# Kernel optimization log

Hardware: AMD Instinct MI355X
Metric: run time of the kernel (lower is better)

The kernel has to match this reference:

```python
import jax, jax.numpy as jnp
import numpy as np

D_MODEL = 512
H = 8
DEPTH = D_MODEL // H
TOPK = 16
TAU_HID = max(4, D_MODEL // 2)  # 256
TAU_EPS = 1e-6
DT = 1.0
T_SCALAR = 1.0  # default t in call()


def setup_inputs() -> dict:
    key = jax.random.key(0)
    ks = jax.random.split(key, 24)
    B, T = 2, 1024
    D2 = 2 * DEPTH

    def w(k, shape, fan_in):
        return jax.random.normal(k, shape, dtype=jnp.float32) / np.sqrt(fan_in)

    inp = {
        "x": jax.random.normal(ks[0], (B, T, D_MODEL), dtype=jnp.float32),
        "Wq": w(ks[1], (D_MODEL, D_MODEL), D_MODEL), "bq": jnp.zeros((D_MODEL,), jnp.float32),
        "Wk": w(ks[2], (D_MODEL, D_MODEL), D_MODEL), "bk": jnp.zeros((D_MODEL,), jnp.float32),
        "Wv": w(ks[3], (D_MODEL, D_MODEL), D_MODEL), "bv": jnp.zeros((D_MODEL,), jnp.float32),
        "Wo": w(ks[4], (D_MODEL, D_MODEL), D_MODEL), "bo": jnp.zeros((D_MODEL,), jnp.float32),
        "Wpi": w(ks[5], (D2, D_MODEL), D2), "bpi": jnp.zeros((D_MODEL,), jnp.float32),
        "Wpo": w(ks[6], (D_MODEL, 1), D_MODEL), "bpo": jnp.zeros((1,), jnp.float32),
        "Wta": w(ks[7], (D2, 1), D2), "bta": jnp.zeros((1,), jnp.float32),
        "Wtb": w(ks[8], (D2, 1), D2), "btb": jnp.zeros((1,), jnp.float32),
        "Wti": w(ks[9], (D2, TAU_HID), D2), "bti": jnp.zeros((TAU_HID,), jnp.float32),
        "Wto": w(ks[10], (TAU_HID, 1), TAU_HID), "bto": jnp.zeros((1,), jnp.float32),
    }
    return inp


def reference(x, Wq, bq, Wk, bk, Wv, bv, Wo, bo,
              Wpi, bpi, Wpo, bpo, Wta, bta, Wtb, btb, Wti, bti, Wto, bto):
    B, T, _ = x.shape

    def split_heads(z):
        return z.reshape(B, T, H, DEPTH).transpose(0, 2, 1, 3)  # [B,H,T,D]

    qh = split_heads(x @ Wq + bq)
    kh = split_heads(x @ Wk + bk)
    vh = split_heads(x @ Wv + bv)

    # top-k pairwise scores (q @ k^T), select K keys per query
    scores = jnp.einsum('bhqd,bhkd->bhqk', qh, kh)  # [B,H,T,T]
    _, idx = jax.lax.top_k(scores, TOPK)            # [B,H,T,K]

    # gather k and v at top-k indices -> [B,H,T,K,D]
    kg = jnp.take_along_axis(kh[:, :, None, :, :], idx[..., None], axis=3)
    vg = jnp.take_along_axis(vh[:, :, None, :, :], idx[..., None], axis=3)

    # per-pair features [q_i ; k_j] -> [B,H,T,K,2D]
    qt = jnp.broadcast_to(qh[:, :, :, None, :], (B, H, T, TOPK, DEPTH))
    pairs = jnp.concatenate([qt, kg], axis=-1)

    # phi: Dense(d_model) -> Dense(1) -> sigmoid
    phi = jax.nn.sigmoid(((pairs @ Wpi + bpi) @ Wpo + bpo)[..., 0])
    # time interpolation: sigmoid(a*t + b)
    t_a = (pairs @ Wta + bta)[..., 0]
    t_b = (pairs @ Wtb + btb)[..., 0]
    t_interp = jax.nn.sigmoid(t_a * T_SCALAR + t_b)
    # tau: Dense(d_model//2) -> Dense(1) -> softplus + eps
    tau = jax.nn.softplus(((pairs @ Wti + bti) @ Wto + bto)[..., 0]) + TAU_EPS

    # mode == 'exact'
    attn_logits = phi / tau * (1.0 - jnp.exp(-tau * t_interp))
    attn = jax.nn.softmax(attn_logits, axis=-1)  # [B,H,T,K]

    out_h = jnp.einsum('bhqk,bhqkd->bhqd', attn, vg) * DT  # [B,H,T,D]
    combined = out_h.transpose(0, 2, 1, 3).reshape(B, T, D_MODEL)
    return combined @ Wo + bo  # return_sequences=True
```

## Files before the change

### kernel.cpp

```cpp
#include <hip/hip_runtime.h>
#include <math.h>

#define BDIM 2
#define TT 1024
#define NH 8
#define HD 64
#define NTOPK 16
#define NBH 16
#define NTOK 16384

__global__ __launch_bounds__(256) void k_collapse64(
    const float* __restrict__ Wpi, const float* __restrict__ bpi,
    const float* __restrict__ Wpo, const float* __restrict__ bpo,
    const float* __restrict__ Wti, const float* __restrict__ bti,
    const float* __restrict__ Wto, const float* __restrict__ bto,
    double* __restrict__ wphid, double* __restrict__ wtaud,
    double* __restrict__ ccd) {
  int tid = threadIdx.x;
  int blk = blockIdx.x;
  if (blk < 16) {
    int r = blk * 16 + (tid >> 4);
    int l = tid & 15;
    double s = 0.;
    if (r < 128) {
      for (int i = 0; i < 32; ++i)
        s += (double)Wpi[r * 512 + l + 16 * i] * (double)Wpo[l + 16 * i];
    } else {
      int rr = r - 128;
      for (int i = 0; i < 16; ++i)
        s += (double)Wti[rr * 256 + l + 16 * i] * (double)Wto[l + 16 * i];
    }
#pragma unroll
    for (int off = 8; off >= 1; off >>= 1) s += __shfl_xor(s, off, 64);
    if (l == 0) {
      if (r < 128) wphid[r] = s;
      else wtaud[r - 128] = s;
    }
  } else {
    int lane = tid & 63;
    if (tid < 64) {
      double p = 0.;
      for (int c = lane; c < 512; c += 64) p += (double)bpi[c] * (double)Wpo[c];
#pragma unroll
      for (int off = 32; off >= 1; off >>= 1) p += __shfl_xor(p, off, 64);
      if (lane == 0) ccd[0] = p + (double)bpo[0];
    } else if (tid < 128) {
      double p = 0.;
      for (int c = lane; c < 256; c += 64) p += (double)bti[c] * (double)Wto[c];
#pragma unroll
      for (int off = 32; off >= 1; off >>= 1) p += __shfl_xor(p, off, 64);
      if (lane == 0) ccd[1] = p + (double)bto[0];
    }
  }
}

__device__ __forceinline__ void gemm_body(
    const float* __restrict__ A, const float* __restrict__ W,
    const float* __restrict__ bias, float* __restrict__ out,
    int bm, int bn, int mode) {
  __shared__ float As[32][68];
  __shared__ float Bs[32][64];
  const int tid = threadIdx.x;
  const int tx = tid & 15;
  const int ty = tid >> 4;
  float acc[4][4] = {{0.f, 0.f, 0.f, 0.f}};
  for (int k0 = 0; k0 < 512; k0 += 32) {
#pragma unroll
    for (int i = 0; i < 2; ++i) {
      int idx = i * 256 + tid;
      int row = idx >> 3;
      int c4 = (idx & 7) << 2;
      float4 av = *(const float4*)&A[(bm + row) * 512 + k0 + c4];
      As[c4 + 0][row] = av.x;
      As[c4 + 1][row] = av.y;
      As[c4 + 2][row] = av.z;
      As[c4 + 3][row] = av.w;
    }
#pragma unroll
    for (int i = 0; i < 2; ++i) {
      int idx = i * 256 + tid;
      int br = idx >> 4;
      int bc = (idx & 15) << 2;
      *(float4*)&Bs[br][bc] = *(const float4*)&W[(k0 + br) * 512 + bn + bc];
    }
    __syncthreads();
#pragma unroll
    for (int kk = 0; kk < 32; ++kk) {
      float4 a = *(const float4*)&As[kk][ty * 4];
      float4 b = *(const float4*)&Bs[kk][tx << 2];
      acc[0][0] = fmaf(a.x, b.x, acc[0][0]);
      acc[0][1] = fmaf(a.x, b.y, acc[0][1]);
      acc[0][2] = fmaf(a.x, b.z, acc[0][2]);
      acc[0][3] = fmaf(a.x, b.w, acc[0][3]);
      acc[1][0] = fmaf(a.y, b.x, acc[1][0]);
      acc[1][1] = fmaf(a.y, b.y, acc[1][1]);
      acc[1][2] = fmaf(a.y, b.z, acc[1][2]);
      acc[1][3] = fmaf(a.y, b.w, acc[1][3]);
      acc[2][0] = fmaf(a.z, b.x, acc[2][0]);
      acc[2][1] = fmaf(a.z, b.y, acc[2][1]);
      acc[2][2] = fmaf(a.z, b.z, acc[2][2]);
      acc[2][3] = fmaf(a.z, b.w, acc[2][3]);
      acc[3][0] = fmaf(a.w, b.x, acc[3][0]);
      acc[3][1] = fmaf(a.w, b.y, acc[3][1]);
      acc[3][2] = fmaf(a.w, b.z, acc[3][2]);
      acc[3][3] = fmaf(a.w, b.w, acc[3][3]);
    }
    __syncthreads();
  }
#pragma unroll
  for (int i = 0; i < 4; ++i) {
    int row = bm + ty * 4 + i;
    float4 r;
    r.x = acc[i][0] + bias[bn + tx * 4 + 0];
    r.y = acc[i][1] + bias[bn + tx * 4 + 1];
    r.z = acc[i][2] + bias[bn + tx * 4 + 2];
    r.w = acc[i][3] + bias[bn + tx * 4 + 3];
    if (mode == 0) {
      *(float4*)&out[row * 512 + bn + tx * 4] = r;
    } else {
      int bb = row >> 10;
      int tt2 = row & 1023;
      int head = bn >> 6;
      *(float4*)&out[(((bb * NH + head) * TT + tt2) << 6) + tx * 4] = r;
    }
  }
}

__global__ __launch_bounds__(256) void k_gemm(
    const float* __restrict__ A, const float* __restrict__ W,
    const float* __restrict__ bias, float* __restrict__ out, int mode) {
  gemm_body(A, W, bias, out, blockIdx.y * 64, blockIdx.x * 64, mode);
}

__global__ __launch_bounds__(256) void k_gemm_qkv(
    const float* __restrict__ A,
    const float* __restrict__ Wq, const float* __restrict__ bq,
    const float* __restrict__ Wk, const float* __restrict__ bk,
    const float* __restrict__ Wv, const float* __restrict__ bv,
    float* __restrict__ Qf, float* __restrict__ Kf, float* __restrict__ Vf) {
  int which = blockIdx.x >> 3;
  int bn = (blockIdx.x & 7) * 64;
  const float* W = (which == 0) ? Wq : (which == 1) ? Wk : Wv;
  const float* b = (which == 0) ? bq : (which == 1) ? bk : bv;
  float* out = (which == 0) ? Qf : (which == 1) ? Kf : Vf;
  gemm_body(A, W, b, out, blockIdx.y * 64, bn, 1);
}

__global__ __launch_bounds__(256) void k_tokscal64(
    const float* __restrict__ Qg, const float* __restrict__ Kg,
    const double* __restrict__ wphid, const float* __restrict__ Wta,
    const float* __restrict__ Wtb, const double* __restrict__ wtaud,
    double4* __restrict__ sqd4, double4* __restrict__ skd4) {
  __shared__ double wp[128], wa[128], wb[128], wt[128];
  int tid = threadIdx.x;
  if (tid < 128) {
    wp[tid] = wphid[tid];
    wa[tid] = (double)Wta[tid];
    wb[tid] = (double)Wtb[tid];
    wt[tid] = wtaud[tid];
  }
  __syncthreads();
  int tok = blockIdx.x * 256 + tid;
  const float* qr = Qg + (size_t)tok * 64;
  const float* kr = Kg + (size_t)tok * 64;
  double sp = 0., sa = 0., sb = 0., st = 0.;
  double kp = 0., ka = 0., kb2 = 0., kt = 0.;
#pragma unroll
  for (int d = 0; d < 64; ++d) {
    double q = (double)qr[d];
    double k = (double)kr[d];
    sp += q * wp[d];
    sa += q * wa[d];
    sb += q * wb[d];
    st += q * wt[d];
    kp += k * wp[64 + d];
    ka += k * wa[64 + d];
    kb2 += k * wb[64 + d];
    kt += k * wt[64 + d];
  }
  sqd4[tok] = make_double4(sp, sa, sb, st);
  skd4[tok] = make_double4(kp, ka, kb2, kt);
}

__global__ __launch_bounds__(256) void k_score(
    const float* __restrict__ Qf, const float* __restrict__ Kf,
    float* __restrict__ Sc) {
  __shared__ float As[32][132];
  __shared__ float Bs[32][132];
  const int bn = blockIdx.x * 128;
  const int bm = blockIdx.y * 128;
  const int bh = blockIdx.z;
  const float* A = Qf + (size_t)bh * (TT * 64);
  const float* K = Kf + (size_t)bh * (TT * 64);
  float* out = Sc + (size_t)bh * (TT * 1024);
  const int tid = threadIdx.x;
  const int tx = tid & 15;
  const int ty = tid >> 4;
  float acc[8][8];
#pragma unroll
  for (int i = 0; i < 8; ++i)
#pragma unroll
    for (int j = 0; j < 8; ++j) acc[i][j] = 0.f;
  for (int k0 = 0; k0 < 64; k0 += 32) {
#pragma unroll
    for (int i = 0; i < 4; ++i) {
      int idx = i * 256 + tid;
      int row = idx >> 3;
      int c4 = (idx & 7) << 2;
      float4 av = *(const float4*)&A[(size_t)(bm + row) * 64 + k0 + c4];
      As[c4 + 0][row] = av.x;
      As[c4 + 1][row] = av.y;
      As[c4 + 2][row] = av.z;
      As[c4 + 3][row] = av.w;
      float4 kv = *(const float4*)&K[(size_t)(bn + row) * 64 + k0 + c4];
      Bs[c4 + 0][row] = kv.x;
      Bs[c4 + 1][row] = kv.y;
      Bs[c4 + 2][row] = kv.z;
      Bs[c4 + 3][row] = kv.w;
    }
    __syncthreads();
#pragma unroll
    for (int kk = 0; kk < 32; ++kk) {
      float4 alo = *(const float4*)&As[kk][ty * 8];
      float4 ahi = *(const float4*)&As[kk][ty * 8 + 4];
      float4 blo = *(const float4*)&Bs[kk][tx * 8];
      float4 bhi = *(const float4*)&Bs[kk][tx * 8 + 4];
      float a[8] = {alo.x, alo.y, alo.z, alo.w, ahi.x, ahi.y, ahi.z, ahi.w};
      float b[8] = {blo.x, blo.y, blo.z, blo.w, bhi.x, bhi.y, bhi.z, bhi.w};
#pragma unroll
      for (int i = 0; i < 8; ++i)
#pragma unroll
        for (int j = 0; j < 8; ++j)
          acc[i][j] = fmaf(a[i], b[j], acc[i][j]);
    }
    __syncthreads();
  }
#pragma unroll
  for (int i = 0; i < 8; ++i) {
    float4 r0 = make_float4(acc[i][0], acc[i][1], acc[i][2], acc[i][3]);
    float4 r1 = make_float4(acc[i][4], acc[i][5], acc[i][6], acc[i][7]);
    size_t base = (size_t)(bm + ty * 8 + i) * 1024 + bn + tx * 8;
    *(float4*)&out[base] = r0;
    *(float4*)&out[base + 4] = r1;
  }
}

__global__ __launch_bounds__(256) void k_topk(
    const float* __restrict__ Sc, const float* __restrict__ Vg,
    const double4* __restrict__ sqd4, const double4* __restrict__ skd4,
    const double* __restrict__ ccd, const float* __restrict__ btaP,
    const float* __restrict__ btbP, float* __restrict__ C) {
  const int tid = threadIdx.x;
  const int lane = tid & 63;
  const int wv = tid >> 6;
  const int qg = blockIdx.x * 4 + wv;
  const int bh = qg >> 10;
  const int qa = qg & 1023;
  const int bb = bh >> 3;
  const int hh = bh & 7;
  const float* rowp = Sc + (size_t)qg * 1024;
  const float* Vbh = Vg + (size_t)bh * (TT * 64);

  float v[16];
#pragma unroll
  for (int j4 = 0; j4 < 4; ++j4) {
    float4 t = *(const float4*)&rowp[j4 * 256 + lane * 4];
    v[j4 * 4 + 0] = t.x;
    v[j4 * 4 + 1] = t.y;
    v[j4 * 4 + 2] = t.z;
    v[j4 * 4 + 3] = t.w;
  }
  float gv[4];
  int gj[4];
#pragma unroll
  for (int g = 0; g < 4; ++g) {
    gv[g] = v[4 * g];
    gj[g] = 4 * g;
#pragma unroll
    for (int e = 1; e < 4; ++e) {
      if (v[4 * g + e] > gv[g]) { gv[g] = v[4 * g + e]; gj[g] = 4 * g + e; }
    }
  }
  int myk = 0;
#pragma unroll 1
  for (int it = 0; it < NTOPK; ++it) {
    float bvv = gv[0];
    int bjj = gj[0];
#pragma unroll
    for (int g = 1; g < 4; ++g) {
      if (gv[g] > bvv) { bvv = gv[g]; bjj = gj[g]; }
    }
    int bj = ((bjj >> 2) << 8) + (lane << 2) + (bjj & 3);
#pragma unroll
    for (int off = 32; off >= 1; off >>= 1) {
      float ov = __shfl_xor(bvv, off, 64);
      int oj = __shfl_xor(bj, off, 64);
      if (ov > bvv || (ov == bvv && oj < bj)) { bvv = ov; bj = oj; }
    }
    if (lane == it) myk = bj;
    int owner = (bj >> 2) & 63;
    int slot = (((bj >> 8) << 2)) | (bj & 3);
    if (lane == owner) {
#pragma unroll
      for (int jj = 0; jj < 16; ++jj)
        if (jj == slot) v[jj] = -INFINITY;
      int g2 = slot >> 2;
#pragma unroll
      for (int g = 0; g < 4; ++g) {
        if (g == g2) {
          float ngv = v[4 * g];
          int ngj = 4 * g;
#pragma unroll
          for (int e = 1; e < 4; ++e) {
            if (v[4 * g + e] > ngv) { ngv = v[4 * g + e]; ngj = 4 * g + e; }
          }
          gv[g] = ngv;
          gj[g] = ngj;
        }
      }
    }
  }
  const double cphi = ccd[0];
  const double ctau = ccd[1];
  const double bta0 = (double)btaP[0];
  const double btb0 = (double)btbP[0];
  double4 sq = sqd4[qg];
  float logit = -INFINITY;
  if (lane < 16) {
    double4 sk = skd4[bh * TT + myk];
    float xs = (float)(sq.x + sk.x + cphi);
    float ta = (float)(sq.y + sk.y + bta0);
    float tb = (float)(sq.z + sk.z + btb0);
    float tl = (float)(sq.w + sk.w + ctau);
    float phi = 1.f / (1.f + __expf(-xs));
    float ti = 1.f / (1.f + __expf(-(ta + tb)));
    float tau = fmaxf(tl, 0.f) + log1pf(__expf(-fabsf(tl))) + 1e-6f;
    logit = phi / tau * (1.f - __expf(-tau * ti));
  }
  float m = logit;
#pragma unroll
  for (int off = 8; off >= 1; off >>= 1) m = fmaxf(m, __shfl_xor(m, off, 64));
  float e = (lane < 16) ? __expf(logit - m) : 0.f;
  float ssum = e;
#pragma unroll
  for (int off = 8; off >= 1; off >>= 1) ssum += __shfl_xor(ssum, off, 64);
  float w = e / ssum;
  float outv = 0.f;
#pragma unroll
  for (int k2 = 0; k2 < NTOPK; ++k2) {
    float wk = __shfl(w, k2, 64);
    int ik = __shfl(myk, k2, 64);
    outv = fmaf(wk, Vbh[(size_t)ik * 64 + lane], outv);
  }
  C[(bb * TT + qa) * 512 + hh * 64 + lane] = outv;
}

__global__ __launch_bounds__(256) void k_attn(
    const float* __restrict__ Qg, const float* __restrict__ Kg,
    const float* __restrict__ Vg, const double4* __restrict__ sqd4,
    const double4* __restrict__ skd4, const double* __restrict__ ccd,
    const float* __restrict__ btaP, const float* __restrict__ btbP,
    float* __restrict__ C) {
  __shared__ float qs[8][64];
  __shared__ float sc[8][1024];
  const int bh = blockIdx.y;
  const int q0 = blockIdx.x * 8;
  const int tid = threadIdx.x;
  const int lane = tid & 63;
  const int wv = tid >> 6;
  if (tid < 128) {
    int q = tid >> 4, d4 = (tid & 15) << 2;
    *(float4*)&qs[q][d4] = *(const float4*)&Qg[(size_t)(bh * TT + q0 + q) * 64 + d4];
  }
  __syncthreads();
#pragma unroll 1
  for (int c = 0; c < 4; ++c) {
    const int kb = (c * 4 + wv) * 64;
    const float* krow = &Kg[(size_t)(bh * TT + kb + lane) * 64];
    float4 kr[16];
#pragma unroll
    for (int i = 0; i < 16; ++i) kr[i] = *(const float4*)&krow[i * 4];
#pragma unroll
    for (int q = 0; q < 8; ++q) {
      float s = 0.f;
#pragma unroll
      for (int i = 0; i < 16; ++i) {
        float4 q4 = *(const float4*)&qs[q][i * 4];
        s = fmaf(q4.x, kr[i].x, s);
        s = fmaf(q4.y, kr[i].y, s);
        s = fmaf(q4.z, kr[i].z, s);
        s = fmaf(q4.w, kr[i].w, s);
      }
      sc[q][kb + lane] = s;
    }
  }
  __syncthreads();
  const double cphi = ccd[0];
  const double ctau = ccd[1];
  const double bta0 = (double)btaP[0];
  const double btb0 = (double)btbP[0];
  const int bb = bh >> 3;
  const int hh = bh & 7;
  const float* Vbh = Vg + (size_t)bh * (TT * 64);
#pragma unroll 1
  for (int qq = 0; qq < 2; ++qq) {
    const int ql = wv * 2 + qq;
    const int qa = q0 + ql;
    const float* rowp = &sc[ql][0];
    float v[16];
#pragma unroll
    for (int jj = 0; jj < 16; ++jj) v[jj] = rowp[jj * 64 + lane];
    float gv[4];
    int gj[4];
#pragma unroll
    for (int g = 0; g < 4; ++g) {
      gv[g] = v[4 * g];
      gj[g] = 4 * g;
#pragma unroll
      for (int e = 1; e < 4; ++e) {
        if (v[4 * g + e] > gv[g]) { gv[g] = v[4 * g + e]; gj[g] = 4 * g + e; }
      }
    }
    int myk = 0;
#pragma unroll 1
    for (int it = 0; it < NTOPK; ++it) {
      float bvv = gv[0];
      int bjj = gj[0];
#pragma unroll
      for (int g = 1; g < 4; ++g) {
        if (gv[g] > bvv) { bvv = gv[g]; bjj = gj[g]; }
      }
      int bj = bjj * 64 + lane;
#pragma unroll
      for (int off = 32; off >= 1; off >>= 1) {
        float ov = __shfl_xor(bvv, off, 64);
        int oj = __shfl_xor(bj, off, 64);
        if (ov > bvv || (ov == bvv && oj < bj)) { bvv = ov; bj = oj; }
      }
      if (lane == it) myk = bj;
      int owner = bj & 63;
      int slot = bj >> 6;
      if (lane == owner) {
#pragma unroll
        for (int jj = 0; jj < 16; ++jj)
          if (jj == slot) v[jj] = -INFINITY;
        int g2 = slot >> 2;
#pragma unroll
        for (int g = 0; g < 4; ++g) {
          if (g == g2) {
            float ngv = v[4 * g];
            int ngj = 4 * g;
#pragma unroll
            for (int e = 1; e < 4; ++e) {
              if (v[4 * g + e] > ngv) { ngv = v[4 * g + e]; ngj = 4 * g + e; }
            }
            gv[g] = ngv;
            gj[g] = ngj;
          }
        }
      }
    }
    double4 sq = sqd4[bh * TT + qa];
    double logit = -INFINITY;
    if (lane < 16) {
      double4 sk = skd4[bh * TT + myk];
      double phi = 1.0 / (1.0 + exp(-(sq.x + sk.x + cphi)));
      double ta = sq.y + sk.y + bta0;
      double tb = sq.z + sk.z + btb0;
      double ti = 1.0 / (1.0 + exp(-(ta * 1.0 + tb)));
      double tl = sq.w + sk.w + ctau;
      double tau = fmax(tl, 0.0) + log1p(exp(-fabs(tl))) + 1e-6;
      logit = phi / tau * (1.0 - exp(-tau * ti));
    }
    double m = logit;
#pragma unroll
    for (int off = 8; off >= 1; off >>= 1) {
      double om = __shfl_xor(m, off, 64);
      m = fmax(m, om);
    }
    double e = (lane < 16) ? exp(logit - m) : 0.0;
    double ssum = e;
#pragma unroll
    for (int off = 8; off >= 1; off >>= 1) ssum += __shfl_xor(ssum, off, 64);
    double w = e / ssum;
    double outv = 0.0;
#pragma unroll
    for (int k2 = 0; k2 < NTOPK; ++k2) {
      double wk = __shfl(w, k2, 64);
      int ik = __shfl(myk, k2, 64);
      outv += wk * (double)Vbh[(size_t)ik * 64 + lane];
    }
    C[(bb * TT + qa) * 512 + hh * 64 + lane] = (float)outv;
  }
}

extern "C" void kernel_launch(void* const* d_in, const int* in_sizes, int n_in,
                              void* d_out, int out_size, void* d_ws, size_t ws_size,
                              hipStream_t stream) {
  (void)in_sizes; (void)n_in; (void)out_size;
  const float* x   = (const float*)d_in[0];
  const float* Wq  = (const float*)d_in[1];
  const float* bq  = (const float*)d_in[2];
  const float* Wk  = (const float*)d_in[3];
  const float* bk  = (const float*)d_in[4];
  const float* Wv  = (const float*)d_in[5];
  const float* bv  = (const float*)d_in[6];
  const float* Wo  = (const float*)d_in[7];
  const float* bo  = (const float*)d_in[8];
  const float* Wpi = (const float*)d_in[9];
  const float* bpi = (const float*)d_in[10];
  const float* Wpo = (const float*)d_in[11];
  const float* bpo = (const float*)d_in[12];
  const float* Wta = (const float*)d_in[13];
  const float* bta = (const float*)d_in[14];
  const float* Wtb = (const float*)d_in[15];
  const float* btb = (const float*)d_in[16];
  const float* Wti = (const float*)d_in[17];
  const float* bti = (const float*)d_in[18];
  const float* Wto = (const float*)d_in[19];
  const float* bto = (const float*)d_in[20];

  double* wsd = (double*)d_ws;
  double4* sqd4 = (double4*)wsd;
  double4* skd4 = (double4*)(wsd + 65536);
  double* wphid = wsd + 131072;
  double* wtaud = wsd + 131200;
  double* ccd   = wsd + 131328;
  float* fs = (float*)(wsd + 131332);
  float* Qf = fs;
  float* Kf = fs + 1048576;
  float* Vf = fs + 2097152;
  float* Cf = fs + 3145728;
  float* Sc = fs + 4194304;
  const size_t need = (size_t)131332 * 8 + (size_t)(4194304 + 16777216) * 4;

  hipLaunchKernelGGL(k_collapse64, dim3(17), dim3(256), 0, stream,
                     Wpi, bpi, Wpo, bpo, Wti, bti, Wto, bto, wphid, wtaud, ccd);
  hipLaunchKernelGGL(k_gemm_qkv, dim3(24, 32), dim3(256), 0, stream,
                     x, Wq, bq, Wk, bk, Wv, bv, Qf, Kf, Vf);
  hipLaunchKernelGGL(k_tokscal64, dim3(NTOK / 256), dim3(256), 0, stream,
                     Qf, Kf, wphid, Wta, Wtb, wtaud, sqd4, skd4);
  if (ws_size >= need) {
    hipLaunchKernelGGL(k_score, dim3(8, 8, 16), dim3(256), 0, stream, Qf, Kf, Sc);
    hipLaunchKernelGGL(k_topk, dim3(NTOK / 4), dim3(256), 0, stream,
                       Sc, Vf, sqd4, skd4, ccd, bta, btb, Cf);
  } else {
    hipLaunchKernelGGL(k_attn, dim3(TT / 8, NBH), dim3(256), 0, stream,
                       Qf, Kf, Vf, sqd4, skd4, ccd, bta, btb, Cf);
  }
  hipLaunchKernelGGL(k_gemm, dim3(8, 32), dim3(256), 0, stream,
                     Cf, Wo, bo, (float*)d_out, 0);
}
```

Measured before the change: 272.8 us.

## Fuse per-tile top-16 candidate selection into score GEMM and merge candidates

The score GEMM no longer writes the full 1024x1024 score matrix per head. Each 128x128 tile now selects its own top-16 candidates per query row with shuffle reductions and writes them out. A second kernel merges the 128 candidates per query into the final top-16, which shrinks score traffic from 64 MB to 8 MB. The token-scalar kernel also moves to 64-thread blocks with float4 loads. The cost is a serial 16-iteration selection loop inside the GEMM epilogue, which adds latency and register pressure.

```diff
diff --git a/kernel.cpp b/kernel.cpp
--- a/kernel.cpp
+++ b/kernel.cpp
@@ -146,45 +146,50 @@
   gemm_body(A, W, b, out, blockIdx.y * 64, bn, 1);
 }
 
-__global__ __launch_bounds__(256) void k_tokscal64(
+__global__ __launch_bounds__(64) void k_tokscal64(
     const float* __restrict__ Qg, const float* __restrict__ Kg,
     const double* __restrict__ wphid, const float* __restrict__ Wta,
     const float* __restrict__ Wtb, const double* __restrict__ wtaud,
     double4* __restrict__ sqd4, double4* __restrict__ skd4) {
   __shared__ double wp[128], wa[128], wb[128], wt[128];
   int tid = threadIdx.x;
-  if (tid < 128) {
-    wp[tid] = wphid[tid];
-    wa[tid] = (double)Wta[tid];
-    wb[tid] = (double)Wtb[tid];
-    wt[tid] = wtaud[tid];
+#pragma unroll
+  for (int h = 0; h < 2; ++h) {
+    int i = h * 64 + tid;
+    wp[i] = wphid[i];
+    wa[i] = (double)Wta[i];
+    wb[i] = (double)Wtb[i];
+    wt[i] = wtaud[i];
   }
   __syncthreads();
-  int tok = blockIdx.x * 256 + tid;
-  const float* qr = Qg + (size_t)tok * 64;
-  const float* kr = Kg + (size_t)tok * 64;
+  int tok = blockIdx.x * 64 + tid;
+  const float4* qr = (const float4*)(Qg + (size_t)tok * 64);
+  const float4* kr = (const float4*)(Kg + (size_t)tok * 64);
   double sp = 0., sa = 0., sb = 0., st = 0.;
   double kp = 0., ka = 0., kb2 = 0., kt = 0.;
 #pragma unroll
-  for (int d = 0; d < 64; ++d) {
-    double q = (double)qr[d];
-    double k = (double)kr[d];
-    sp += q * wp[d];
-    sa += q * wa[d];
-    sb += q * wb[d];
-    st += q * wt[d];
-    kp += k * wp[64 + d];
-    ka += k * wa[64 + d];
-    kb2 += k * wb[64 + d];
-    kt += k * wt[64 + d];
+  for (int i = 0; i < 16; ++i) {
+    float4 qv = qr[i];
+    float4 kv = kr[i];
+    double q0 = (double)qv.x, q1 = (double)qv.y, q2 = (double)qv.z, q3 = (double)qv.w;
+    double k0 = (double)kv.x, k1 = (double)kv.y, k2 = (double)kv.z, k3 = (double)kv.w;
+    int d = i * 4;
+    sp += q0 * wp[d]; sp += q1 * wp[d + 1]; sp += q2 * wp[d + 2]; sp += q3 * wp[d + 3];
+    sa += q0 * wa[d]; sa += q1 * wa[d + 1]; sa += q2 * wa[d + 2]; sa += q3 * wa[d + 3];
+    sb += q0 * wb[d]; sb += q1 * wb[d + 1]; sb += q2 * wb[d + 2]; sb += q3 * wb[d + 3];
+    st += q0 * wt[d]; st += q1 * wt[d + 1]; st += q2 * wt[d + 2]; st += q3 * wt[d + 3];
+    kp += k0 * wp[64 + d]; kp += k1 * wp[64 + d + 1]; kp += k2 * wp[64 + d + 2]; kp += k3 * wp[64 + d + 3];
+    ka += k0 * wa[64 + d]; ka += k1 * wa[64 + d + 1]; ka += k2 * wa[64 + d + 2]; ka += k3 * wa[64 + d + 3];
+    kb2 += k0 * wb[64 + d]; kb2 += k1 * wb[64 + d + 1]; kb2 += k2 * wb[64 + d + 2]; kb2 += k3 * wb[64 + d + 3];
+    kt += k0 * wt[64 + d]; kt += k1 * wt[64 + d + 1]; kt += k2 * wt[64 + d + 2]; kt += k3 * wt[64 + d + 3];
   }
   sqd4[tok] = make_double4(sp, sa, sb, st);
   skd4[tok] = make_double4(kp, ka, kb2, kt);
 }
 
-__global__ __launch_bounds__(256) void k_score(
+__global__ __launch_bounds__(256) void k_score_sel(
     const float* __restrict__ Qf, const float* __restrict__ Kf,
-    float* __restrict__ Sc) {
+    float* __restrict__ CandV, int* __restrict__ CandI) {
   __shared__ float As[32][132];
   __shared__ float Bs[32][132];
   const int bn = blockIdx.x * 128;
@@ -192,7 +197,6 @@
   const int bh = blockIdx.z;
   const float* A = Qf + (size_t)bh * (TT * 64);
   const float* K = Kf + (size_t)bh * (TT * 64);
-  float* out = Sc + (size_t)bh * (TT * 1024);
   const int tid = threadIdx.x;
   const int tx = tid & 15;
   const int ty = tid >> 4;
@@ -235,21 +239,52 @@
     }
     __syncthreads();
   }
-#pragma unroll
+  const int t = blockIdx.x;
+#pragma unroll 1
   for (int i = 0; i < 8; ++i) {
-    float4 r0 = make_float4(acc[i][0], acc[i][1], acc[i][2], acc[i][3]);
-    float4 r1 = make_float4(acc[i][4], acc[i][5], acc[i][6], acc[i][7]);
-    size_t base = (size_t)(bm + ty * 8 + i) * 1024 + bn + tx * 8;
-    *(float4*)&out[base] = r0;
-    *(float4*)&out[base + 4] = r1;
-  }
-}
-
-__global__ __launch_bounds__(256) void k_topk(
-    const float* __restrict__ Sc, const float* __restrict__ Vg,
-    const double4* __restrict__ sqd4, const double4* __restrict__ skd4,
-    const double* __restrict__ ccd, const float* __restrict__ btaP,
-    const float* __restrict__ btbP, float* __restrict__ C) {
+    float tv[8];
+#pragma unroll
+    for (int j = 0; j < 8; ++j) tv[j] = acc[i][j];
+    float lb = tv[0];
+    int lj = 0;
+#pragma unroll
+    for (int j = 1; j < 8; ++j)
+      if (tv[j] > lb) { lb = tv[j]; lj = j; }
+    float wvv = 0.f;
+    int wii = 0;
+#pragma unroll 1
+    for (int it = 0; it < NTOPK; ++it) {
+      float bv = lb;
+      int bidx = bn + tx * 8 + lj;
+#pragma unroll
+      for (int off = 8; off >= 1; off >>= 1) {
+        float ov = __shfl_xor(bv, off, 64);
+        int oi = __shfl_xor(bidx, off, 64);
+        if (ov > bv || (ov == bv && oi < bidx)) { bv = ov; bidx = oi; }
+      }
+      if (tx == it) { wvv = bv; wii = bidx; }
+      int rel = bidx - bn;
+      if (tx == (rel >> 3)) {
+        tv[rel & 7] = -INFINITY;
+        lb = tv[0];
+        lj = 0;
+#pragma unroll
+        for (int j = 1; j < 8; ++j)
+          if (tv[j] > lb) { lb = tv[j]; lj = j; }
+      }
+    }
+    size_t qg = (size_t)bh * TT + bm + ty * 8 + i;
+    CandV[qg * 128 + t * 16 + tx] = wvv;
+    CandI[qg * 128 + t * 16 + tx] = wii;
+  }
+}
+
+__global__ __launch_bounds__(256) void k_topk2(
+    const float* __restrict__ CandV, const int* __restrict__ CandI,
+    const float* __restrict__ Vg, const double4* __restrict__ sqd4,
+    const double4* __restrict__ skd4, const double* __restrict__ ccd,
+    const float* __restrict__ btaP, const float* __restrict__ btbP,
+    float* __restrict__ C) {
   const int tid = threadIdx.x;
   const int lane = tid & 63;
   const int wv = tid >> 6;
@@ -258,67 +293,27 @@
   const int qa = qg & 1023;
   const int bb = bh >> 3;
   const int hh = bh & 7;
-  const float* rowp = Sc + (size_t)qg * 1024;
   const float* Vbh = Vg + (size_t)bh * (TT * 64);
 
-  float v[16];
-#pragma unroll
-  for (int j4 = 0; j4 < 4; ++j4) {
-    float4 t = *(const float4*)&rowp[j4 * 256 + lane * 4];
-    v[j4 * 4 + 0] = t.x;
-    v[j4 * 4 + 1] = t.y;
-    v[j4 * 4 + 2] = t.z;
-    v[j4 * 4 + 3] = t.w;
-  }
-  float gv[4];
-  int gj[4];
-#pragma unroll
-  for (int g = 0; g < 4; ++g) {
-    gv[g] = v[4 * g];
-    gj[g] = 4 * g;
-#pragma unroll
-    for (int e = 1; e < 4; ++e) {
-      if (v[4 * g + e] > gv[g]) { gv[g] = v[4 * g + e]; gj[g] = 4 * g + e; }
-    }
-  }
+  float v0 = CandV[(size_t)qg * 128 + lane];
+  float v1 = CandV[(size_t)qg * 128 + 64 + lane];
+  int i0 = CandI[(size_t)qg * 128 + lane];
+  int i1 = CandI[(size_t)qg * 128 + 64 + lane];
   int myk = 0;
 #pragma unroll 1
   for (int it = 0; it < NTOPK; ++it) {
-    float bvv = gv[0];
-    int bjj = gj[0];
-#pragma unroll
-    for (int g = 1; g < 4; ++g) {
-      if (gv[g] > bvv) { bvv = gv[g]; bjj = gj[g]; }
-    }
-    int bj = ((bjj >> 2) << 8) + (lane << 2) + (bjj & 3);
+    bool f = (v0 > v1) || (v0 == v1 && i0 < i1);
+    float bv = f ? v0 : v1;
+    int bidx = f ? i0 : i1;
 #pragma unroll
     for (int off = 32; off >= 1; off >>= 1) {
-      float ov = __shfl_xor(bvv, off, 64);
-      int oj = __shfl_xor(bj, off, 64);
-      if (ov > bvv || (ov == bvv && oj < bj)) { bvv = ov; bj = oj; }
-    }
-    if (lane == it) myk = bj;
-    int owner = (bj >> 2) & 63;
-    int slot = (((bj >> 8) << 2)) | (bj & 3);
-    if (lane == owner) {
-#pragma unroll
-      for (int jj = 0; jj < 16; ++jj)
-        if (jj == slot) v[jj] = -INFINITY;
-      int g2 = slot >> 2;
-#pragma unroll
-      for (int g = 0; g < 4; ++g) {
-        if (g == g2) {
-          float ngv = v[4 * g];
-          int ngj = 4 * g;
-#pragma unroll
-          for (int e = 1; e < 4; ++e) {
-            if (v[4 * g + e] > ngv) { ngv = v[4 * g + e]; ngj = 4 * g + e; }
-          }
-          gv[g] = ngv;
-          gj[g] = ngj;
-        }
-      }
-    }
+      float ov = __shfl_xor(bv, off, 64);
+      int oi = __shfl_xor(bidx, off, 64);
+      if (ov > bv || (ov == bv && oi < bidx)) { bv = ov; bidx = oi; }
+    }
+    if (lane == it) myk = bidx;
+    if (i0 == bidx) v0 = -INFINITY;
+    if (i1 == bidx) v1 = -INFINITY;
   }
   const double cphi = ccd[0];
   const double ctau = ccd[1];
@@ -531,19 +526,21 @@
   float* Kf = fs + 1048576;
   float* Vf = fs + 2097152;
   float* Cf = fs + 3145728;
-  float* Sc = fs + 4194304;
-  const size_t need = (size_t)131332 * 8 + (size_t)(4194304 + 16777216) * 4;
+  float* CandV = fs + 4194304;
+  int*   CandI = (int*)(fs + 6291456);
+  const size_t need = (size_t)131332 * 8 + (size_t)(4194304 + 4194304) * 4;
 
   hipLaunchKernelGGL(k_collapse64, dim3(17), dim3(256), 0, stream,
                      Wpi, bpi, Wpo, bpo, Wti, bti, Wto, bto, wphid, wtaud, ccd);
   hipLaunchKernelGGL(k_gemm_qkv, dim3(24, 32), dim3(256), 0, stream,
                      x, Wq, bq, Wk, bk, Wv, bv, Qf, Kf, Vf);
-  hipLaunchKernelGGL(k_tokscal64, dim3(NTOK / 256), dim3(256), 0, stream,
+  hipLaunchKernelGGL(k_tokscal64, dim3(NTOK / 64), dim3(64), 0, stream,
                      Qf, Kf, wphid, Wta, Wtb, wtaud, sqd4, skd4);
   if (ws_size >= need) {
-    hipLaunchKernelGGL(k_score, dim3(8, 8, 16), dim3(256), 0, stream, Qf, Kf, Sc);
-    hipLaunchKernelGGL(k_topk, dim3(NTOK / 4), dim3(256), 0, stream,
-                       Sc, Vf, sqd4, skd4, ccd, bta, btb, Cf);
+    hipLaunchKernelGGL(k_score_sel, dim3(8, 8, 16), dim3(256), 0, stream,
+                       Qf, Kf, CandV, CandI);
+    hipLaunchKernelGGL(k_topk2, dim3(NTOK / 4), dim3(256), 0, stream,
+                       CandV, CandI, Vf, sqd4, skd4, ccd, bta, btb, Cf);
   } else {
     hipLaunchKernelGGL(k_attn, dim3(TT / 8, NBH), dim3(256), 0, stream,
                        Qf, Kf, Vf, sqd4, skd4, ccd, bta, btb, Cf);
```

After: 398.6 us. +46.1%, slower.

## Process two query rows per wave in top-k, enlarge GEMM K-tile, shrink tokscal blocks

Applied to the files above, without the earlier changes.

The top-k kernel now has each wavefront handle two query rows at once, interleaving their selection loops, shuffles and V gathers. The aim is more independent work per wave to hide shuffle and memory latency, and half as many blocks. The GEMM K-tile doubles from 32 to 64, which halves barrier and loop overhead but doubles shared memory. The token-scalar kernel moves to 64-thread blocks with float4 loads to spread work over more CUs. The trade-off is higher register pressure in top-k, which may lower occupancy.

```diff
diff --git a/kernel.cpp b/kernel.cpp
--- a/kernel.cpp
+++ b/kernel.cpp
@@ -58,18 +58,18 @@
     const float* __restrict__ A, const float* __restrict__ W,
     const float* __restrict__ bias, float* __restrict__ out,
     int bm, int bn, int mode) {
-  __shared__ float As[32][68];
-  __shared__ float Bs[32][64];
+  __shared__ float As[64][68];
+  __shared__ float Bs[64][64];
   const int tid = threadIdx.x;
   const int tx = tid & 15;
   const int ty = tid >> 4;
   float acc[4][4] = {{0.f, 0.f, 0.f, 0.f}};
-  for (int k0 = 0; k0 < 512; k0 += 32) {
-#pragma unroll
-    for (int i = 0; i < 2; ++i) {
+  for (int k0 = 0; k0 < 512; k0 += 64) {
+#pragma unroll
+    for (int i = 0; i < 4; ++i) {
       int idx = i * 256 + tid;
-      int row = idx >> 3;
-      int c4 = (idx & 7) << 2;
+      int row = idx >> 4;
+      int c4 = (idx & 15) << 2;
       float4 av = *(const float4*)&A[(bm + row) * 512 + k0 + c4];
       As[c4 + 0][row] = av.x;
       As[c4 + 1][row] = av.y;
@@ -77,7 +77,7 @@
       As[c4 + 3][row] = av.w;
     }
 #pragma unroll
-    for (int i = 0; i < 2; ++i) {
+    for (int i = 0; i < 4; ++i) {
       int idx = i * 256 + tid;
       int br = idx >> 4;
       int bc = (idx & 15) << 2;
@@ -85,7 +85,7 @@
     }
     __syncthreads();
 #pragma unroll
-    for (int kk = 0; kk < 32; ++kk) {
+    for (int kk = 0; kk < 64; ++kk) {
       float4 a = *(const float4*)&As[kk][ty * 4];
       float4 b = *(const float4*)&Bs[kk][tx << 2];
       acc[0][0] = fmaf(a.x, b.x, acc[0][0]);
@@ -146,37 +146,42 @@
   gemm_body(A, W, b, out, blockIdx.y * 64, bn, 1);
 }
 
-__global__ __launch_bounds__(256) void k_tokscal64(
+__global__ __launch_bounds__(64) void k_tokscal64(
     const float* __restrict__ Qg, const float* __restrict__ Kg,
     const double* __restrict__ wphid, const float* __restrict__ Wta,
     const float* __restrict__ Wtb, const double* __restrict__ wtaud,
     double4* __restrict__ sqd4, double4* __restrict__ skd4) {
   __shared__ double wp[128], wa[128], wb[128], wt[128];
   int tid = threadIdx.x;
-  if (tid < 128) {
-    wp[tid] = wphid[tid];
-    wa[tid] = (double)Wta[tid];
-    wb[tid] = (double)Wtb[tid];
-    wt[tid] = wtaud[tid];
+#pragma unroll
+  for (int h = 0; h < 2; ++h) {
+    int i = h * 64 + tid;
+    wp[i] = wphid[i];
+    wa[i] = (double)Wta[i];
+    wb[i] = (double)Wtb[i];
+    wt[i] = wtaud[i];
   }
   __syncthreads();
-  int tok = blockIdx.x * 256 + tid;
-  const float* qr = Qg + (size_t)tok * 64;
-  const float* kr = Kg + (size_t)tok * 64;
+  int tok = blockIdx.x * 64 + tid;
+  const float4* qr = (const float4*)(Qg + (size_t)tok * 64);
+  const float4* kr = (const float4*)(Kg + (size_t)tok * 64);
   double sp = 0., sa = 0., sb = 0., st = 0.;
   double kp = 0., ka = 0., kb2 = 0., kt = 0.;
 #pragma unroll
-  for (int d = 0; d < 64; ++d) {
-    double q = (double)qr[d];
-    double k = (double)kr[d];
-    sp += q * wp[d];
-    sa += q * wa[d];
-    sb += q * wb[d];
-    st += q * wt[d];
-    kp += k * wp[64 + d];
-    ka += k * wa[64 + d];
-    kb2 += k * wb[64 + d];
-    kt += k * wt[64 + d];
+  for (int i = 0; i < 16; ++i) {
+    float4 qv = qr[i];
+    float4 kv = kr[i];
+    double q0 = (double)qv.x, q1 = (double)qv.y, q2 = (double)qv.z, q3 = (double)qv.w;
+    double k0 = (double)kv.x, k1 = (double)kv.y, k2 = (double)kv.z, k3 = (double)kv.w;
+    int d = i * 4;
+    sp += q0 * wp[d]; sp += q1 * wp[d + 1]; sp += q2 * wp[d + 2]; sp += q3 * wp[d + 3];
+    sa += q0 * wa[d]; sa += q1 * wa[d + 1]; sa += q2 * wa[d + 2]; sa += q3 * wa[d + 3];
+    sb += q0 * wb[d]; sb += q1 * wb[d + 1]; sb += q2 * wb[d + 2]; sb += q3 * wb[d + 3];
+    st += q0 * wt[d]; st += q1 * wt[d + 1]; st += q2 * wt[d + 2]; st += q3 * wt[d + 3];
+    kp += k0 * wp[64 + d]; kp += k1 * wp[64 + d + 1]; kp += k2 * wp[64 + d + 2]; kp += k3 * wp[64 + d + 3];
+    ka += k0 * wa[64 + d]; ka += k1 * wa[64 + d + 1]; ka += k2 * wa[64 + d + 2]; ka += k3 * wa[64 + d + 3];
+    kb2 += k0 * wb[64 + d]; kb2 += k1 * wb[64 + d + 1]; kb2 += k2 * wb[64 + d + 2]; kb2 += k3 * wb[64 + d + 3];
+    kt += k0 * wt[64 + d]; kt += k1 * wt[64 + d + 1]; kt += k2 * wt[64 + d + 2]; kt += k3 * wt[64 + d + 3];
   }
   sqd4[tok] = make_double4(sp, sa, sb, st);
   skd4[tok] = make_double4(kp, ka, kb2, kt);
@@ -253,69 +258,102 @@
   const int tid = threadIdx.x;
   const int lane = tid & 63;
   const int wv = tid >> 6;
-  const int qg = blockIdx.x * 4 + wv;
-  const int bh = qg >> 10;
-  const int qa = qg & 1023;
+  const int qA = blockIdx.x * 8 + wv * 2;
+  const int qB = qA + 1;
+  const int bh = qA >> 10;
   const int bb = bh >> 3;
   const int hh = bh & 7;
-  const float* rowp = Sc + (size_t)qg * 1024;
+  const float* rA = Sc + (size_t)qA * 1024;
+  const float* rB = Sc + (size_t)qB * 1024;
   const float* Vbh = Vg + (size_t)bh * (TT * 64);
 
-  float v[16];
+  float vA[16], vB[16];
 #pragma unroll
   for (int j4 = 0; j4 < 4; ++j4) {
-    float4 t = *(const float4*)&rowp[j4 * 256 + lane * 4];
-    v[j4 * 4 + 0] = t.x;
-    v[j4 * 4 + 1] = t.y;
-    v[j4 * 4 + 2] = t.z;
-    v[j4 * 4 + 3] = t.w;
-  }
-  float gv[4];
-  int gj[4];
+    float4 tA = *(const float4*)&rA[j4 * 256 + lane * 4];
+    float4 tB = *(const float4*)&rB[j4 * 256 + lane * 4];
+    vA[j4 * 4 + 0] = tA.x; vA[j4 * 4 + 1] = tA.y;
+    vA[j4 * 4 + 2] = tA.z; vA[j4 * 4 + 3] = tA.w;
+    vB[j4 * 4 + 0] = tB.x; vB[j4 * 4 + 1] = tB.y;
+    vB[j4 * 4 + 2] = tB.z; vB[j4 * 4 + 3] = tB.w;
+  }
+  float gvA[4], gvB[4];
+  int gjA[4], gjB[4];
 #pragma unroll
   for (int g = 0; g < 4; ++g) {
-    gv[g] = v[4 * g];
-    gj[g] = 4 * g;
+    gvA[g] = vA[4 * g]; gjA[g] = 4 * g;
+    gvB[g] = vB[4 * g]; gjB[g] = 4 * g;
 #pragma unroll
     for (int e = 1; e < 4; ++e) {
-      if (v[4 * g + e] > gv[g]) { gv[g] = v[4 * g + e]; gj[g] = 4 * g + e; }
-    }
-  }
-  int myk = 0;
+      if (vA[4 * g + e] > gvA[g]) { gvA[g] = vA[4 * g + e]; gjA[g] = 4 * g + e; }
+      if (vB[4 * g + e] > gvB[g]) { gvB[g] = vB[4 * g + e]; gjB[g] = 4 * g + e; }
+    }
+  }
+  int mykA = 0, mykB = 0;
 #pragma unroll 1
   for (int it = 0; it < NTOPK; ++it) {
-    float bvv = gv[0];
-    int bjj = gj[0];
+    float bvA = gvA[0], bvB = gvB[0];
+    int bjjA = gjA[0], bjjB = gjB[0];
 #pragma unroll
     for (int g = 1; g < 4; ++g) {
-      if (gv[g] > bvv) { bvv = gv[g]; bjj = gj[g]; }
-    }
-    int bj = ((bjj >> 2) << 8) + (lane << 2) + (bjj & 3);
+      if (gvA[g] > bvA) { bvA = gvA[g]; bjjA = gjA[g]; }
+      if (gvB[g] > bvB) { bvB = gvB[g]; bjjB = gjB[g]; }
+    }
+    int bjA = ((bjjA >> 2) << 8) + (lane << 2) + (bjjA & 3);
+    int bjB = ((bjjB >> 2) << 8) + (lane << 2) + (bjjB & 3);
 #pragma unroll
     for (int off = 32; off >= 1; off >>= 1) {
-      float ov = __shfl_xor(bvv, off, 64);
-      int oj = __shfl_xor(bj, off, 64);
-      if (ov > bvv || (ov == bvv && oj < bj)) { bvv = ov; bj = oj; }
-    }
-    if (lane == it) myk = bj;
-    int owner = (bj >> 2) & 63;
-    int slot = (((bj >> 8) << 2)) | (bj & 3);
-    if (lane == owner) {
-#pragma unroll
-      for (int jj = 0; jj < 16; ++jj)
-        if (jj == slot) v[jj] = -INFINITY;
-      int g2 = slot >> 2;
-#pragma unroll
-      for (int g = 0; g < 4; ++g) {
-        if (g == g2) {
-          float ngv = v[4 * g];
-          int ngj = 4 * g;
-#pragma unroll
-          for (int e = 1; e < 4; ++e) {
-            if (v[4 * g + e] > ngv) { ngv = v[4 * g + e]; ngj = 4 * g + e; }
+      float ovA = __shfl_xor(bvA, off, 64);
+      int ojA = __shfl_xor(bjA, off, 64);
+      float ovB = __shfl_xor(bvB, off, 64);
+      int ojB = __shfl_xor(bjB, off, 64);
+      if (ovA > bvA || (ovA == bvA && ojA < bjA)) { bvA = ovA; bjA = ojA; }
+      if (ovB > bvB || (ovB == bvB && ojB < bjB)) { bvB = ovB; bjB = ojB; }
+    }
+    if (lane == it) { mykA = bjA; mykB = bjB; }
+    {
+      int owner = (bjA >> 2) & 63;
+      int slot = ((bjA >> 8) << 2) | (bjA & 3);
+      if (lane == owner) {
+#pragma unroll
+        for (int jj = 0; jj < 16; ++jj)
+          if (jj == slot) vA[jj] = -INFINITY;
+        int g2 = slot >> 2;
+#pragma unroll
+        for (int g = 0; g < 4; ++g) {
+          if (g == g2) {
+            float ngv = vA[4 * g];
+            int ngj = 4 * g;
+#pragma unroll
+            for (int e = 1; e < 4; ++e) {
+              if (vA[4 * g + e] > ngv) { ngv = vA[4 * g + e]; ngj = 4 * g + e; }
+            }
+            gvA[g] = ngv;
+            gjA[g] = ngj;
           }
-          gv[g] = ngv;
-          gj[g] = ngj;
+        }
+      }
+    }
+    {
+      int owner = (bjB >> 2) & 63;
+      int slot = ((bjB >> 8) << 2) | (bjB & 3);
+      if (lane == owner) {
+#pragma unroll
+        for (int jj = 0; jj < 16; ++jj)
+          if (jj == slot) vB[jj] = -INFINITY;
+        int g2 = slot >> 2;
+#pragma unroll
+        for (int g = 0; g < 4; ++g) {
+          if (g == g2) {
+            float ngv = vB[4 * g];
+            int ngj = 4 * g;
+#pragma unroll
+            for (int e = 1; e < 4; ++e) {
+              if (vB[4 * g + e] > ngv) { ngv = vB[4 * g + e]; ngj = 4 * g + e; }
+            }
+            gvB[g] = ngv;
+            gjB[g] = ngj;
+          }
         }
       }
     }
@@ -324,35 +362,58 @@
   const double ctau = ccd[1];
   const double bta0 = (double)btaP[0];
   const double btb0 = (double)btbP[0];
-  double4 sq = sqd4[qg];
-  float logit = -INFINITY;
+  double4 sqA = sqd4[qA];
+  double4 sqB = sqd4[qB];
+  float logitA = -INFINITY, logitB = -INFINITY;
   if (lane < 16) {
-    double4 sk = skd4[bh * TT + myk];
-    float xs = (float)(sq.x + sk.x + cphi);
-    float ta = (float)(sq.y + sk.y + bta0);
-    float tb = (float)(sq.z + sk.z + btb0);
-    float tl = (float)(sq.w + sk.w + ctau);
-    float phi = 1.f / (1.f + __expf(-xs));
-    float ti = 1.f / (1.f + __expf(-(ta + tb)));
-    float tau = fmaxf(tl, 0.f) + log1pf(__expf(-fabsf(tl))) + 1e-6f;
-    logit = phi / tau * (1.f - __expf(-tau * ti));
-  }
-  float m = logit;
-#pragma unroll
-  for (int off = 8; off >= 1; off >>= 1) m = fmaxf(m, __shfl_xor(m, off, 64));
-  float e = (lane < 16) ? __expf(logit - m) : 0.f;
-  float ssum = e;
-#pragma unroll
-  for (int off = 8; off >= 1; off >>= 1) ssum += __shfl_xor(ssum, off, 64);
-  float w = e / ssum;
-  float outv = 0.f;
+    double4 skA = skd4[bh * TT + mykA];
+    double4 skB = skd4[bh * TT + mykB];
+    float xsA = (float)(sqA.x + skA.x + cphi);
+    float taA = (float)(sqA.y + skA.y + bta0);
+    float tbA = (float)(sqA.z + skA.z + btb0);
+    float tlA = (float)(sqA.w + skA.w + ctau);
+    float xsB = (float)(sqB.x + skB.x + cphi);
+    float taB = (float)(sqB.y + skB.y + bta0);
+    float tbB = (float)(sqB.z + skB.z + btb0);
+    float tlB = (float)(sqB.w + skB.w + ctau);
+    float phiA = 1.f / (1.f + __expf(-xsA));
+    float tiA = 1.f / (1.f + __expf(-(taA + tbA)));
+    float tauA = fmaxf(tlA, 0.f) + log1pf(__expf(-fabsf(tlA))) + 1e-6f;
+    logitA = phiA / tauA * (1.f - __expf(-tauA * tiA));
+    float phiB = 1.f / (1.f + __expf(-xsB));
+    float tiB = 1.f / (1.f + __expf(-(taB + tbB)));
+    float tauB = fmaxf(tlB, 0.f) + log1pf(__expf(-fabsf(tlB))) + 1e-6f;
+    logitB = phiB / tauB * (1.f - __expf(-tauB * tiB));
+  }
+  float mA = logitA, mB = logitB;
+#pragma unroll
+  for (int off = 8; off >= 1; off >>= 1) {
+    mA = fmaxf(mA, __shfl_xor(mA, off, 64));
+    mB = fmaxf(mB, __shfl_xor(mB, off, 64));
+  }
+  float eA = (lane < 16) ? __expf(logitA - mA) : 0.f;
+  float eB = (lane < 16) ? __expf(logitB - mB) : 0.f;
+  float sA = eA, sB = eB;
+#pragma unroll
+  for (int off = 8; off >= 1; off >>= 1) {
+    sA += __shfl_xor(sA, off, 64);
+    sB += __shfl_xor(sB, off, 64);
+  }
+  float wA = eA / sA;
+  float wB = eB / sB;
+  float outA = 0.f, outB = 0.f;
 #pragma unroll
   for (int k2 = 0; k2 < NTOPK; ++k2) {
-    float wk = __shfl(w, k2, 64);
-    int ik = __shfl(myk, k2, 64);
-    outv = fmaf(wk, Vbh[(size_t)ik * 64 + lane], outv);
-  }
-  C[(bb * TT + qa) * 512 + hh * 64 + lane] = outv;
+    float wkA = __shfl(wA, k2, 64);
+    int ikA = __shfl(mykA, k2, 64);
+    float wkB = __shfl(wB, k2, 64);
+    int ikB = __shfl(mykB, k2, 64);
+    outA = fmaf(wkA, Vbh[(size_t)ikA * 64 + lane], outA);
+    outB = fmaf(wkB, Vbh[(size_t)ikB * 64 + lane], outB);
+  }
+  const int qaA = qA & 1023;
+  C[(bb * TT + qaA) * 512 + hh * 64 + lane] = outA;
+  C[(bb * TT + qaA + 1) * 512 + hh * 64 + lane] = outB;
 }
 
 __global__ __launch_bounds__(256) void k_attn(
@@ -538,11 +599,11 @@
                      Wpi, bpi, Wpo, bpo, Wti, bti, Wto, bto, wphid, wtaud, ccd);
   hipLaunchKernelGGL(k_gemm_qkv, dim3(24, 32), dim3(256), 0, stream,
                      x, Wq, bq, Wk, bk, Wv, bv, Qf, Kf, Vf);
-  hipLaunchKernelGGL(k_tokscal64, dim3(NTOK / 256), dim3(256), 0, stream,
+  hipLaunchKernelGGL(k_tokscal64, dim3(NTOK / 64), dim3(64), 0, stream,
                      Qf, Kf, wphid, Wta, Wtb, wtaud, sqd4, skd4);
   if (ws_size >= need) {
     hipLaunchKernelGGL(k_score, dim3(8, 8, 16), dim3(256), 0, stream, Qf, Kf, Sc);
-    hipLaunchKernelGGL(k_topk, dim3(NTOK / 4), dim3(256), 0, stream,
+    hipLaunchKernelGGL(k_topk, dim3(NTOK / 8), dim3(256), 0, stream,
                        Sc, Vf, sqd4, skd4, ccd, bta, btb, Cf);
   } else {
     hipLaunchKernelGGL(k_attn, dim3(TT / 8, NBH), dim3(256), 0, stream,
```

Result: no change. 274.4 us (+0.6%).
